# Performance work log

Hardware: AMD Instinct MI355X
Metric: run time of the kernel (lower is better)

Reference implementation:

```python
import jax, jax.numpy as jnp
import numpy as np

BSZ, L, D = 64, 128, 2048


def setup_inputs() -> dict:
    key = jax.random.key(0)
    k1, k2, k3 = jax.random.split(key, 3)
    encoder_output = jax.random.normal(k1, (BSZ, L, D), dtype=jnp.float32)
    # ragged turn lengths in [2, L]; prefix mask like torch turn_lengths = mask.sum(1)
    lengths = jax.random.randint(k2, (BSZ,), 2, L + 1)
    mask = (jnp.arange(L)[None, :] < lengths[:, None]).astype(jnp.int32)
    W = jax.random.normal(k3, (2 * D, 2), dtype=jnp.float32) * (1.0 / np.sqrt(2 * D))
    b = jnp.zeros((2,), dtype=jnp.float32)
    return {"encoder_output": encoder_output, "mask": mask, "W": W, "b": b}


def reference(encoder_output, mask, W, b):
    bsz, max_len, d = encoder_output.shape
    turn_lengths = jnp.sum(mask, axis=1)  # [bsz]
    # con_fc(concat(h_j, h_k)) == h_j @ W[:d] + h_k @ W[d:] + b  (exact split of the linear)
    left = jnp.einsum('bld,dc->blc', encoder_output, W[:d])   # [b, L, 2]
    right = jnp.einsum('bld,dc->blc', encoder_output, W[d:])  # [b, L, 2]
    logits = left[:, :, None, :] + right[:, None, :, :] + b   # [b, L(j), L(k), 2]
    j = jnp.arange(max_len)[:, None]
    k = jnp.arange(max_len)[None, :]
    # pairs gathered by torch loops: k < j < turn_lengths[i]; label 1 iff k == j-1
    valid = (k < j) & (j < turn_lengths[:, None, None])        # [b, L, L]
    labels = (k == j - 1).astype(jnp.int32)                    # [L, L]
    logp = jax.nn.log_softmax(logits, axis=-1)                 # [b, L, L, 2]
    nll = -jnp.take_along_axis(
        logp, jnp.broadcast_to(labels[None, :, :, None], (bsz, max_len, max_len, 1)), axis=-1
    )[..., 0]                                                  # [b, L, L]
    n_valid = jnp.sum(valid)
    dli_loss = jnp.sum(jnp.where(valid, nll, 0.0)) / jnp.maximum(n_valid, 1).astype(nll.dtype)
    return dli_loss
```

## Files before the change

### kernel.cpp

```cpp
#include <hip/hip_runtime.h>

#define BSZ 64
#define LMAX 128
#define DIM 2048
#define NPOS (BSZ * LMAX)

struct Ctrl {
    float accum;
    int   count;
    int   done2;
};

__global__ __launch_bounds__(512, 6) void proj_kernel(
        const float* __restrict__ enc,
        const float* __restrict__ W,
        float* __restrict__ proj,
        Ctrl* __restrict__ ctrl) {
    if (blockIdx.x == 0 && threadIdx.x == 0) {
        ctrl->accum = 0.f; ctrl->count = 0; ctrl->done2 = 0;
    }

    const int tid  = threadIdx.x;
    const int wid  = tid >> 6;
    const int lane = tid & 63;
    const int quad = wid >> 2;
    const int qw   = wid & 3;
    const int p0   = (blockIdx.x * 2 + quad) * 4;

    const float4* __restrict__ W4 = (const float4*)W;
    float4 wl0[2], wl1[2], wr0[2], wr1[2];
    #pragma unroll
    for (int it = 0; it < 2; ++it) {
        const int idx = qw * 128 + it * 64 + lane;
        wl0[it] = W4[idx * 2];
        wl1[it] = W4[idx * 2 + 1];
        wr0[it] = W4[1024 + idx * 2];
        wr1[it] = W4[1024 + idx * 2 + 1];
    }

    const float4* __restrict__ h4 = (const float4*)enc;
    const size_t base = (size_t)p0 * (DIM / 4) + qw * 128 + lane;

    float4 hA0 = h4[base];
    float4 hA1 = h4[base + 64];

    float* __restrict__ projf = proj + (size_t)qw * NPOS * 4;

    #pragma unroll
    for (int q = 0; q < 4; ++q) {
        float4 hB0, hB1;
        if (q < 3) {
            const size_t nb = base + (size_t)(q + 1) * (DIM / 4);
            hB0 = h4[nb];
            hB1 = h4[nb + 64];
        }
        float a0, a1, a2, a3;
        a0 = hA0.x * wl0[0].x + hA0.y * wl0[0].z + hA0.z * wl1[0].x + hA0.w * wl1[0].z
           + hA1.x * wl0[1].x + hA1.y * wl0[1].z + hA1.z * wl1[1].x + hA1.w * wl1[1].z;
        a1 = hA0.x * wl0[0].y + hA0.y * wl0[0].w + hA0.z * wl1[0].y + hA0.w * wl1[0].w
           + hA1.x * wl0[1].y + hA1.y * wl0[1].w + hA1.z * wl1[1].y + hA1.w * wl1[1].w;
        a2 = hA0.x * wr0[0].x + hA0.y * wr0[0].z + hA0.z * wr1[0].x + hA0.w * wr1[0].z
           + hA1.x * wr0[1].x + hA1.y * wr0[1].z + hA1.z * wr1[1].x + hA1.w * wr1[1].z;
        a3 = hA0.x * wr0[0].y + hA0.y * wr0[0].w + hA0.z * wr1[0].y + hA0.w * wr1[0].w
           + hA1.x * wr0[1].y + hA1.y * wr0[1].w + hA1.z * wr1[1].y + hA1.w * wr1[1].w;

        const bool o1 = (lane & 1);
        const float r1 = __shfl_xor(o1 ? a0 : a1, 1);
        float s = (o1 ? a1 : a0) + r1;
        const float r2 = __shfl_xor(o1 ? a2 : a3, 1);
        float t = (o1 ? a3 : a2) + r2;
        const bool o2 = (lane & 2);
        const float r3 = __shfl_xor(o2 ? s : t, 2);
        float u = (o2 ? t : s) + r3;
        u += __shfl_xor(u, 4);
        u += __shfl_xor(u, 8);
        u += __shfl_xor(u, 16);
        u += __shfl_xor(u, 32);
        if (lane < 4) projf[(size_t)(p0 + q) * 4 + lane] = u;

        if (q < 3) { hA0 = hB0; hA1 = hB1; }
    }
}

__global__ __launch_bounds__(256) void loss_kernel(
        const int* __restrict__ mask,
        const float* __restrict__ proj,
        const float* __restrict__ bias,
        Ctrl* __restrict__ ctrl,
        float* __restrict__ out) {
    __shared__ float4 s_proj[LMAX];
    __shared__ float  s_w[4];
    __shared__ int    s_m[4];

    const int b   = blockIdx.x >> 2;
    const int q   = blockIdx.x & 3;
    const int tid = threadIdx.x;

    const float4* proj4 = (const float4*)proj;
    if (tid < LMAX) {
        const float4 pa = proj4[0 * NPOS + b * LMAX + tid];
        const float4 pb = proj4[1 * NPOS + b * LMAX + tid];
        const float4 pc = proj4[2 * NPOS + b * LMAX + tid];
        const float4 pd = proj4[3 * NPOS + b * LMAX + tid];
        float4 v;
        v.x = (pa.x + pb.x) + (pc.x + pd.x);
        v.y = (pa.y + pb.y) + (pc.y + pd.y);
        v.z = (pa.z + pb.z) + (pc.z + pd.z);
        v.w = (pa.w + pb.w) + (pc.w + pd.w);
        s_proj[tid] = v;
    }

    int m = (tid < LMAX) ? mask[b * LMAX + tid] : 0;
    #pragma unroll
    for (int off = 32; off >= 1; off >>= 1) m += __shfl_xor(m, off);
    if ((tid & 63) == 0) s_m[tid >> 6] = m;
    __syncthreads();

    const int   T  = s_m[0] + s_m[1] + s_m[2] + s_m[3];
    const float b0 = bias[0];
    const float b1 = bias[1];

    float local = 0.f;
    const int tmax = T << 7;
    for (int t = q * 256 + tid; t < tmax; t += 1024) {
        const int j = t >> 7;
        const int k = t & (LMAX - 1);
        if (k < j) {
            const float4 pj = s_proj[j];
            const float4 pk = s_proj[k];
            const float l0 = pj.x + pk.z + b0;
            const float l1 = pj.y + pk.w + b1;
            const bool  pos = (k == j - 1);
            const float d  = pos ? (l0 - l1) : (l1 - l0);
            local += fmaxf(d, 0.f) + __logf(1.f + __expf(-fabsf(d)));
        }
    }

    #pragma unroll
    for (int off = 32; off >= 1; off >>= 1) local += __shfl_xor(local, off);
    if ((tid & 63) == 0) s_w[tid >> 6] = local;
    __syncthreads();

    if (tid == 0) {
        atomicAdd(&ctrl->accum, s_w[0] + s_w[1] + s_w[2] + s_w[3]);
        if (q == 0) atomicAdd(&ctrl->count, T * (T - 1) / 2);
        __threadfence();
        const int prev = atomicAdd(&ctrl->done2, 1);
        if (prev == 4 * BSZ - 1) {
            const float s = atomicAdd(&ctrl->accum, 0.0f);
            const int   c = atomicAdd(&ctrl->count, 0);
            out[0] = s / (float)(c > 1 ? c : 1);
        }
    }
}

extern "C" void kernel_launch(void* const* d_in, const int* in_sizes, int n_in,
                              void* d_out, int out_size, void* d_ws, size_t ws_size,
                              hipStream_t stream) {
    const float* enc  = (const float*)d_in[0];
    const int*   mask = (const int*)d_in[1];
    const float* W    = (const float*)d_in[2];
    const float* bias = (const float*)d_in[3];
    float* out = (float*)d_out;

    float* proj = (float*)d_ws;
    Ctrl*  ctrl = (Ctrl*)((char*)d_ws + 4 * NPOS * 16);

    proj_kernel<<<NPOS / 8, 512, 0, stream>>>(enc, W, proj, ctrl);
    loss_kernel<<<4 * BSZ, 256, 0, stream>>>(mask, proj, bias, ctrl, out);
}
```

Baseline: 26.93 us.

## Fuse projection and loss into one kernel with per-batch completion flags

Merges the projection and loss kernels into a single launch. The first 1024 blocks compute projections and bump a per-batch counter; 64 tail blocks (one per batch, 512 threads) spin on their batch's counter and then compute the loss. A tiny init kernel zeroes the control block, so there are still two launches. The aim is to overlap the loss with projection work and avoid the gap between kernels. The spin-wait depends on block scheduling order, since tail blocks have higher indices, and the loss work per block grows as it drops from four blocks per batch to one.

```diff
diff --git a/kernel.cpp b/kernel.cpp
--- a/kernel.cpp
+++ b/kernel.cpp
@@ -4,97 +4,115 @@
 #define LMAX 128
 #define DIM 2048
 #define NPOS (BSZ * LMAX)
+#define NPROJ_BLOCKS 1024
+#define NTAIL BSZ
 
 struct Ctrl {
     float accum;
     int   count;
     int   done2;
+    int   pad[13];
+    int   done[BSZ * 16];
 };
 
-__global__ __launch_bounds__(512, 6) void proj_kernel(
+__global__ void init_kernel(Ctrl* __restrict__ ctrl) {
+    int* p = (int*)ctrl;
+    const int n = sizeof(Ctrl) / 4;
+    for (int i = threadIdx.x; i < n; i += 256) p[i] = 0;
+}
+
+__global__ __launch_bounds__(512, 6) void fused_kernel(
         const float* __restrict__ enc,
         const float* __restrict__ W,
+        const int* __restrict__ mask,
+        const float* __restrict__ bias,
         float* __restrict__ proj,
-        Ctrl* __restrict__ ctrl) {
-    if (blockIdx.x == 0 && threadIdx.x == 0) {
-        ctrl->accum = 0.f; ctrl->count = 0; ctrl->done2 = 0;
+        Ctrl* __restrict__ ctrl,
+        float* __restrict__ out) {
+    const int tid = threadIdx.x;
+
+    if (blockIdx.x < NPROJ_BLOCKS) {
+        const int wid  = tid >> 6;
+        const int lane = tid & 63;
+        const int quad = wid >> 2;
+        const int qw   = wid & 3;
+        const int p0   = (blockIdx.x * 2 + quad) * 4;
+
+        const float4* __restrict__ W4 = (const float4*)W;
+        float4 wl0[2], wl1[2], wr0[2], wr1[2];
+        #pragma unroll
+        for (int it = 0; it < 2; ++it) {
+            const int idx = qw * 128 + it * 64 + lane;
+            wl0[it] = W4[idx * 2];
+            wl1[it] = W4[idx * 2 + 1];
+            wr0[it] = W4[1024 + idx * 2];
+            wr1[it] = W4[1024 + idx * 2 + 1];
+        }
+
+        const float4* __restrict__ h4 = (const float4*)enc;
+        const size_t base = (size_t)p0 * (DIM / 4) + qw * 128 + lane;
+
+        float4 hA0 = h4[base];
+        float4 hA1 = h4[base + 64];
+
+        float* __restrict__ projf = proj + (size_t)qw * NPOS * 4;
+
+        #pragma unroll
+        for (int q = 0; q < 4; ++q) {
+            float4 hB0, hB1;
+            if (q < 3) {
+                const size_t nb = base + (size_t)(q + 1) * (DIM / 4);
+                hB0 = h4[nb];
+                hB1 = h4[nb + 64];
+            }
+            float a0, a1, a2, a3;
+            a0 = hA0.x * wl0[0].x + hA0.y * wl0[0].z + hA0.z * wl1[0].x + hA0.w * wl1[0].z
+               + hA1.x * wl0[1].x + hA1.y * wl0[1].z + hA1.z * wl1[1].x + hA1.w * wl1[1].z;
+            a1 = hA0.x * wl0[0].y + hA0.y * wl0[0].w + hA0.z * wl1[0].y + hA0.w * wl1[0].w
+               + hA1.x * wl0[1].y + hA1.y * wl0[1].w + hA1.z * wl1[1].y + hA1.w * wl1[1].w;
+            a2 = hA0.x * wr0[0].x + hA0.y * wr0[0].z + hA0.z * wr1[0].x + hA0.w * wr1[0].z
+               + hA1.x * wr0[1].x + hA1.y * wr0[1].z + hA1.z * wr1[1].x + hA1.w * wr1[1].z;
+            a3 = hA0.x * wr0[0].y + hA0.y * wr0[0].w + hA0.z * wr1[0].y + hA0.w * wr1[0].w
+               + hA1.x * wr0[1].y + hA1.y * wr0[1].w + hA1.z * wr1[1].y + hA1.w * wr1[1].w;
+
+            const bool o1 = (lane & 1);
+            const float r1 = __shfl_xor(o1 ? a0 : a1, 1);
+            float s = (o1 ? a1 : a0) + r1;
+            const float r2 = __shfl_xor(o1 ? a2 : a3, 1);
+            float t = (o1 ? a3 : a2) + r2;
+            const bool o2 = (lane & 2);
+            const float r3 = __shfl_xor(o2 ? s : t, 2);
+            float u = (o2 ? t : s) + r3;
+            u += __shfl_xor(u, 4);
+            u += __shfl_xor(u, 8);
+            u += __shfl_xor(u, 16);
+            u += __shfl_xor(u, 32);
+            if (lane < 4) projf[(size_t)(p0 + q) * 4 + lane] = u;
+
+            if (q < 3) { hA0 = hB0; hA1 = hB1; }
+        }
+
+        __syncthreads();
+        if (tid == 0) {
+            __threadfence();
+            atomicAdd(&ctrl->done[(blockIdx.x >> 4) * 16], 1);
+        }
+        return;
     }
 
-    const int tid  = threadIdx.x;
-    const int wid  = tid >> 6;
+    __shared__ float4 s_proj[LMAX];
+    __shared__ float  s_w[8];
+    __shared__ int    s_m[8];
+
+    const int b    = blockIdx.x - NPROJ_BLOCKS;
     const int lane = tid & 63;
-    const int quad = wid >> 2;
-    const int qw   = wid & 3;
-    const int p0   = (blockIdx.x * 2 + quad) * 4;
 
-    const float4* __restrict__ W4 = (const float4*)W;
-    float4 wl0[2], wl1[2], wr0[2], wr1[2];
-    #pragma unroll
-    for (int it = 0; it < 2; ++it) {
-        const int idx = qw * 128 + it * 64 + lane;
-        wl0[it] = W4[idx * 2];
-        wl1[it] = W4[idx * 2 + 1];
-        wr0[it] = W4[1024 + idx * 2];
-        wr1[it] = W4[1024 + idx * 2 + 1];
+    if (tid == 0) {
+        while (atomicAdd(&ctrl->done[b * 16], 0) < 16)
+            __builtin_amdgcn_s_sleep(1);
+        __threadfence();
     }
-
-    const float4* __restrict__ h4 = (const float4*)enc;
-    const size_t base = (size_t)p0 * (DIM / 4) + qw * 128 + lane;
-
-    float4 hA0 = h4[base];
-    float4 hA1 = h4[base + 64];
-
-    float* __restrict__ projf = proj + (size_t)qw * NPOS * 4;
-
-    #pragma unroll
-    for (int q = 0; q < 4; ++q) {
-        float4 hB0, hB1;
-        if (q < 3) {
-            const size_t nb = base + (size_t)(q + 1) * (DIM / 4);
-            hB0 = h4[nb];
-            hB1 = h4[nb + 64];
-        }
-        float a0, a1, a2, a3;
-        a0 = hA0.x * wl0[0].x + hA0.y * wl0[0].z + hA0.z * wl1[0].x + hA0.w * wl1[0].z
-           + hA1.x * wl0[1].x + hA1.y * wl0[1].z + hA1.z * wl1[1].x + hA1.w * wl1[1].z;
-        a1 = hA0.x * wl0[0].y + hA0.y * wl0[0].w + hA0.z * wl1[0].y + hA0.w * wl1[0].w
-           + hA1.x * wl0[1].y + hA1.y * wl0[1].w + hA1.z * wl1[1].y + hA1.w * wl1[1].w;
-        a2 = hA0.x * wr0[0].x + hA0.y * wr0[0].z + hA0.z * wr1[0].x + hA0.w * wr1[0].z
-           + hA1.x * wr0[1].x + hA1.y * wr0[1].z + hA1.z * wr1[1].x + hA1.w * wr1[1].z;
-        a3 = hA0.x * wr0[0].y + hA0.y * wr0[0].w + hA0.z * wr1[0].y + hA0.w * wr1[0].w
-           + hA1.x * wr0[1].y + hA1.y * wr0[1].w + hA1.z * wr1[1].y + hA1.w * wr1[1].w;
-
-        const bool o1 = (lane & 1);
-        const float r1 = __shfl_xor(o1 ? a0 : a1, 1);
-        float s = (o1 ? a1 : a0) + r1;
-        const float r2 = __shfl_xor(o1 ? a2 : a3, 1);
-        float t = (o1 ? a3 : a2) + r2;
-        const bool o2 = (lane & 2);
-        const float r3 = __shfl_xor(o2 ? s : t, 2);
-        float u = (o2 ? t : s) + r3;
-        u += __shfl_xor(u, 4);
-        u += __shfl_xor(u, 8);
-        u += __shfl_xor(u, 16);
-        u += __shfl_xor(u, 32);
-        if (lane < 4) projf[(size_t)(p0 + q) * 4 + lane] = u;
-
-        if (q < 3) { hA0 = hB0; hA1 = hB1; }
-    }
-}
-
-__global__ __launch_bounds__(256) void loss_kernel(
-        const int* __restrict__ mask,
-        const float* __restrict__ proj,
-        const float* __restrict__ bias,
-        Ctrl* __restrict__ ctrl,
-        float* __restrict__ out) {
-    __shared__ float4 s_proj[LMAX];
-    __shared__ float  s_w[4];
-    __shared__ int    s_m[4];
-
-    const int b   = blockIdx.x >> 2;
-    const int q   = blockIdx.x & 3;
-    const int tid = threadIdx.x;
+    __syncthreads();
 
     const float4* proj4 = (const float4*)proj;
     if (tid < LMAX) {
@@ -113,16 +131,18 @@
     int m = (tid < LMAX) ? mask[b * LMAX + tid] : 0;
     #pragma unroll
     for (int off = 32; off >= 1; off >>= 1) m += __shfl_xor(m, off);
-    if ((tid & 63) == 0) s_m[tid >> 6] = m;
+    if (lane == 0) s_m[tid >> 6] = m;
     __syncthreads();
 
-    const int   T  = s_m[0] + s_m[1] + s_m[2] + s_m[3];
+    int T = 0;
+    #pragma unroll
+    for (int w = 0; w < 8; ++w) T += s_m[w];
     const float b0 = bias[0];
     const float b1 = bias[1];
 
     float local = 0.f;
     const int tmax = T << 7;
-    for (int t = q * 256 + tid; t < tmax; t += 1024) {
+    for (int t = tid; t < tmax; t += 512) {
         const int j = t >> 7;
         const int k = t & (LMAX - 1);
         if (k < j) {
@@ -138,18 +158,21 @@
 
     #pragma unroll
     for (int off = 32; off >= 1; off >>= 1) local += __shfl_xor(local, off);
-    if ((tid & 63) == 0) s_w[tid >> 6] = local;
+    if (lane == 0) s_w[tid >> 6] = local;
     __syncthreads();
 
     if (tid == 0) {
-        atomicAdd(&ctrl->accum, s_w[0] + s_w[1] + s_w[2] + s_w[3]);
-        if (q == 0) atomicAdd(&ctrl->count, T * (T - 1) / 2);
+        float s = 0.f;
+        #pragma unroll
+        for (int w = 0; w < 8; ++w) s += s_w[w];
+        atomicAdd(&ctrl->accum, s);
+        atomicAdd(&ctrl->count, T * (T - 1) / 2);
         __threadfence();
         const int prev = atomicAdd(&ctrl->done2, 1);
-        if (prev == 4 * BSZ - 1) {
-            const float s = atomicAdd(&ctrl->accum, 0.0f);
-            const int   c = atomicAdd(&ctrl->count, 0);
-            out[0] = s / (float)(c > 1 ? c : 1);
+        if (prev == NTAIL - 1) {
+            const float sum = atomicAdd(&ctrl->accum, 0.0f);
+            const int   c   = atomicAdd(&ctrl->count, 0);
+            out[0] = sum / (float)(c > 1 ? c : 1);
         }
     }
 }
@@ -166,6 +189,7 @@
     float* proj = (float*)d_ws;
     Ctrl*  ctrl = (Ctrl*)((char*)d_ws + 4 * NPOS * 16);
 
-    proj_kernel<<<NPOS / 8, 512, 0, stream>>>(enc, W, proj, ctrl);
-    loss_kernel<<<4 * BSZ, 256, 0, stream>>>(mask, proj, bias, ctrl, out);
+    init_kernel<<<1, 256, 0, stream>>>(ctrl);
+    fused_kernel<<<NPROJ_BLOCKS + NTAIL, 512, 0, stream>>>(
+        enc, W, mask, bias, proj, ctrl, out);
 }
```

Result: slower. 64.64 us (+140.0%).

## Fuse projection and loss into one per-batch kernel with shared-memory partials

Applied to the files above, without the earlier changes.

Merges the projection and pairwise-loss kernels into a single kernel with one 1024-thread block per batch row. Per-position projections go into shared memory, so the global proj workspace and the second launch are gone, and control reset moves to a hipMemsetAsync. In exchange, only 64 blocks run on a many-CU GPU. Each wave also walks 32 rows serially with single-step prefetch, which may limit memory parallelism for streaming the 64 MB input.

```diff
diff --git a/kernel.cpp b/kernel.cpp
--- a/kernel.cpp
+++ b/kernel.cpp
@@ -3,7 +3,6 @@
 #define BSZ 64
 #define LMAX 128
 #define DIM 2048
-#define NPOS (BSZ * LMAX)
 
 struct Ctrl {
     float accum;
@@ -11,21 +10,24 @@
     int   done2;
 };
 
-__global__ __launch_bounds__(512, 6) void proj_kernel(
+__global__ __launch_bounds__(1024) void mono_kernel(
         const float* __restrict__ enc,
         const float* __restrict__ W,
-        float* __restrict__ proj,
-        Ctrl* __restrict__ ctrl) {
-    if (blockIdx.x == 0 && threadIdx.x == 0) {
-        ctrl->accum = 0.f; ctrl->count = 0; ctrl->done2 = 0;
-    }
+        const int* __restrict__ mask,
+        const float* __restrict__ bias,
+        Ctrl* __restrict__ ctrl,
+        float* __restrict__ out) {
+    __shared__ float  s_part[4][LMAX][4];
+    __shared__ float4 s_proj[LMAX];
+    __shared__ float  s_w[16];
+    __shared__ int    s_m[2];
 
+    const int b    = blockIdx.x;
     const int tid  = threadIdx.x;
     const int wid  = tid >> 6;
     const int lane = tid & 63;
-    const int quad = wid >> 2;
+    const int g    = wid >> 2;
     const int qw   = wid & 3;
-    const int p0   = (blockIdx.x * 2 + quad) * 4;
 
     const float4* __restrict__ W4 = (const float4*)W;
     float4 wl0[2], wl1[2], wr0[2], wr1[2];
@@ -38,18 +40,23 @@
         wr1[it] = W4[1024 + idx * 2 + 1];
     }
 
+    if (tid < LMAX) {
+        int m = mask[b * LMAX + tid];
+        #pragma unroll
+        for (int off = 32; off >= 1; off >>= 1) m += __shfl_xor(m, off);
+        if (lane == 0) s_m[wid] = m;
+    }
+
     const float4* __restrict__ h4 = (const float4*)enc;
-    const size_t base = (size_t)p0 * (DIM / 4) + qw * 128 + lane;
+    const int    pl0  = g * 32;
+    const size_t base = ((size_t)(b * LMAX + pl0)) * (DIM / 4) + qw * 128 + lane;
 
     float4 hA0 = h4[base];
     float4 hA1 = h4[base + 64];
 
-    float* __restrict__ projf = proj + (size_t)qw * NPOS * 4;
-
-    #pragma unroll
-    for (int q = 0; q < 4; ++q) {
+    for (int q = 0; q < 32; ++q) {
         float4 hB0, hB1;
-        if (q < 3) {
+        if (q < 31) {
             const size_t nb = base + (size_t)(q + 1) * (DIM / 4);
             hB0 = h4[nb];
             hB1 = h4[nb + 64];
@@ -76,53 +83,33 @@
         u += __shfl_xor(u, 8);
         u += __shfl_xor(u, 16);
         u += __shfl_xor(u, 32);
-        if (lane < 4) projf[(size_t)(p0 + q) * 4 + lane] = u;
+        if (lane < 4) s_part[qw][pl0 + q][lane] = u;
 
-        if (q < 3) { hA0 = hB0; hA1 = hB1; }
+        if (q < 31) { hA0 = hB0; hA1 = hB1; }
     }
-}
+    __syncthreads();
 
-__global__ __launch_bounds__(256) void loss_kernel(
-        const int* __restrict__ mask,
-        const float* __restrict__ proj,
-        const float* __restrict__ bias,
-        Ctrl* __restrict__ ctrl,
-        float* __restrict__ out) {
-    __shared__ float4 s_proj[LMAX];
-    __shared__ float  s_w[4];
-    __shared__ int    s_m[4];
-
-    const int b   = blockIdx.x >> 2;
-    const int q   = blockIdx.x & 3;
-    const int tid = threadIdx.x;
-
-    const float4* proj4 = (const float4*)proj;
     if (tid < LMAX) {
-        const float4 pa = proj4[0 * NPOS + b * LMAX + tid];
-        const float4 pb = proj4[1 * NPOS + b * LMAX + tid];
-        const float4 pc = proj4[2 * NPOS + b * LMAX + tid];
-        const float4 pd = proj4[3 * NPOS + b * LMAX + tid];
         float4 v;
-        v.x = (pa.x + pb.x) + (pc.x + pd.x);
-        v.y = (pa.y + pb.y) + (pc.y + pd.y);
-        v.z = (pa.z + pb.z) + (pc.z + pd.z);
-        v.w = (pa.w + pb.w) + (pc.w + pd.w);
+        const float4 p0 = *(const float4*)s_part[0][tid];
+        const float4 p1 = *(const float4*)s_part[1][tid];
+        const float4 p2 = *(const float4*)s_part[2][tid];
+        const float4 p3 = *(const float4*)s_part[3][tid];
+        v.x = (p0.x + p1.x) + (p2.x + p3.x);
+        v.y = (p0.y + p1.y) + (p2.y + p3.y);
+        v.z = (p0.z + p1.z) + (p2.z + p3.z);
+        v.w = (p0.w + p1.w) + (p2.w + p3.w);
         s_proj[tid] = v;
     }
-
-    int m = (tid < LMAX) ? mask[b * LMAX + tid] : 0;
-    #pragma unroll
-    for (int off = 32; off >= 1; off >>= 1) m += __shfl_xor(m, off);
-    if ((tid & 63) == 0) s_m[tid >> 6] = m;
     __syncthreads();
 
-    const int   T  = s_m[0] + s_m[1] + s_m[2] + s_m[3];
+    const int   T  = s_m[0] + s_m[1];
     const float b0 = bias[0];
     const float b1 = bias[1];
 
     float local = 0.f;
     const int tmax = T << 7;
-    for (int t = q * 256 + tid; t < tmax; t += 1024) {
+    for (int t = tid; t < tmax; t += 1024) {
         const int j = t >> 7;
         const int k = t & (LMAX - 1);
         if (k < j) {
@@ -135,21 +122,23 @@
             local += fmaxf(d, 0.f) + __logf(1.f + __expf(-fabsf(d)));
         }
     }
-
     #pragma unroll
     for (int off = 32; off >= 1; off >>= 1) local += __shfl_xor(local, off);
-    if ((tid & 63) == 0) s_w[tid >> 6] = local;
+    if (lane == 0) s_w[wid] = local;
     __syncthreads();
 
     if (tid == 0) {
-        atomicAdd(&ctrl->accum, s_w[0] + s_w[1] + s_w[2] + s_w[3]);
-        if (q == 0) atomicAdd(&ctrl->count, T * (T - 1) / 2);
+        float s = 0.f;
+        #pragma unroll
+        for (int w = 0; w < 16; ++w) s += s_w[w];
+        atomicAdd(&ctrl->accum, s);
+        atomicAdd(&ctrl->count, T * (T - 1) / 2);
         __threadfence();
         const int prev = atomicAdd(&ctrl->done2, 1);
-        if (prev == 4 * BSZ - 1) {
-            const float s = atomicAdd(&ctrl->accum, 0.0f);
-            const int   c = atomicAdd(&ctrl->count, 0);
-            out[0] = s / (float)(c > 1 ? c : 1);
+        if (prev == BSZ - 1) {
+            const float sum = atomicAdd(&ctrl->accum, 0.0f);
+            const int   c   = atomicAdd(&ctrl->count, 0);
+            out[0] = sum / (float)(c > 1 ? c : 1);
         }
     }
 }
@@ -163,9 +152,8 @@
     const float* bias = (const float*)d_in[3];
     float* out = (float*)d_out;
 
-    float* proj = (float*)d_ws;
-    Ctrl*  ctrl = (Ctrl*)((char*)d_ws + 4 * NPOS * 16);
+    Ctrl* ctrl = (Ctrl*)d_ws;
 
-    proj_kernel<<<NPOS / 8, 512, 0, stream>>>(enc, W, proj, ctrl);
-    loss_kernel<<<4 * BSZ, 256, 0, stream>>>(mask, proj, bias, ctrl, out);
+    hipMemsetAsync(ctrl, 0, sizeof(Ctrl), stream);
+    mono_kernel<<<BSZ, 1024, 0, stream>>>(enc, W, mask, bias, ctrl, out);
 }
```

Measured after the change: 30.03 us. 11.5% more time.

## Split projection reduction across eight wave slices, issue all row loads upfront

Applied to the files above, without the earlier changes.

Each wave now covers one 256-wide slice of the hidden dimension across all eight positions of the block, instead of four waves per four positions. All eight row loads are issued before any compute, which raises memory-level parallelism per thread. The partial projections grow from four to eight per position, so the loss kernel sums eight partials and the workspace doubles. Register use rises from holding eight float4 rows, and the launch-bounds occupancy hint drops from 6 to 4 blocks per CU.

```diff
diff --git a/kernel.cpp b/kernel.cpp
--- a/kernel.cpp
+++ b/kernel.cpp
@@ -11,7 +11,7 @@
     int   done2;
 };
 
-__global__ __launch_bounds__(512, 6) void proj_kernel(
+__global__ __launch_bounds__(512, 4) void proj_kernel(
         const float* __restrict__ enc,
         const float* __restrict__ W,
         float* __restrict__ proj,
@@ -21,48 +21,32 @@
     }
 
     const int tid  = threadIdx.x;
-    const int wid  = tid >> 6;
+    const int e    = tid >> 6;
     const int lane = tid & 63;
-    const int quad = wid >> 2;
-    const int qw   = wid & 3;
-    const int p0   = (blockIdx.x * 2 + quad) * 4;
+    const int p0   = blockIdx.x * 8;
+    const int idx  = e * 64 + lane;
 
     const float4* __restrict__ W4 = (const float4*)W;
-    float4 wl0[2], wl1[2], wr0[2], wr1[2];
-    #pragma unroll
-    for (int it = 0; it < 2; ++it) {
-        const int idx = qw * 128 + it * 64 + lane;
-        wl0[it] = W4[idx * 2];
-        wl1[it] = W4[idx * 2 + 1];
-        wr0[it] = W4[1024 + idx * 2];
-        wr1[it] = W4[1024 + idx * 2 + 1];
-    }
+    const float4 wl0 = W4[idx * 2];
+    const float4 wl1 = W4[idx * 2 + 1];
+    const float4 wr0 = W4[1024 + idx * 2];
+    const float4 wr1 = W4[1024 + idx * 2 + 1];
 
     const float4* __restrict__ h4 = (const float4*)enc;
-    const size_t base = (size_t)p0 * (DIM / 4) + qw * 128 + lane;
+    const size_t base = (size_t)p0 * (DIM / 4) + idx;
+    float4 h[8];
+    #pragma unroll
+    for (int p = 0; p < 8; ++p) h[p] = h4[base + (size_t)p * (DIM / 4)];
 
-    float4 hA0 = h4[base];
-    float4 hA1 = h4[base + 64];
-
-    float* __restrict__ projf = proj + (size_t)qw * NPOS * 4;
+    float* __restrict__ projf = proj + (size_t)e * NPOS * 4;
 
     #pragma unroll
-    for (int q = 0; q < 4; ++q) {
-        float4 hB0, hB1;
-        if (q < 3) {
-            const size_t nb = base + (size_t)(q + 1) * (DIM / 4);
-            hB0 = h4[nb];
-            hB1 = h4[nb + 64];
-        }
-        float a0, a1, a2, a3;
-        a0 = hA0.x * wl0[0].x + hA0.y * wl0[0].z + hA0.z * wl1[0].x + hA0.w * wl1[0].z
-           + hA1.x * wl0[1].x + hA1.y * wl0[1].z + hA1.z * wl1[1].x + hA1.w * wl1[1].z;
-        a1 = hA0.x * wl0[0].y + hA0.y * wl0[0].w + hA0.z * wl1[0].y + hA0.w * wl1[0].w
-           + hA1.x * wl0[1].y + hA1.y * wl0[1].w + hA1.z * wl1[1].y + hA1.w * wl1[1].w;
-        a2 = hA0.x * wr0[0].x + hA0.y * wr0[0].z + hA0.z * wr1[0].x + hA0.w * wr1[0].z
-           + hA1.x * wr0[1].x + hA1.y * wr0[1].z + hA1.z * wr1[1].x + hA1.w * wr1[1].z;
-        a3 = hA0.x * wr0[0].y + hA0.y * wr0[0].w + hA0.z * wr1[0].y + hA0.w * wr1[0].w
-           + hA1.x * wr0[1].y + hA1.y * wr0[1].w + hA1.z * wr1[1].y + hA1.w * wr1[1].w;
+    for (int p = 0; p < 8; ++p) {
+        const float4 hp = h[p];
+        float a0 = hp.x * wl0.x + hp.y * wl0.z + hp.z * wl1.x + hp.w * wl1.z;
+        float a1 = hp.x * wl0.y + hp.y * wl0.w + hp.z * wl1.y + hp.w * wl1.w;
+        float a2 = hp.x * wr0.x + hp.y * wr0.z + hp.z * wr1.x + hp.w * wr1.z;
+        float a3 = hp.x * wr0.y + hp.y * wr0.w + hp.z * wr1.y + hp.w * wr1.w;
 
         const bool o1 = (lane & 1);
         const float r1 = __shfl_xor(o1 ? a0 : a1, 1);
@@ -76,9 +60,7 @@
         u += __shfl_xor(u, 8);
         u += __shfl_xor(u, 16);
         u += __shfl_xor(u, 32);
-        if (lane < 4) projf[(size_t)(p0 + q) * 4 + lane] = u;
-
-        if (q < 3) { hA0 = hB0; hA1 = hB1; }
+        if (lane < 4) projf[(size_t)(p0 + p) * 4 + lane] = u;
     }
 }
 
@@ -98,15 +80,13 @@
 
     const float4* proj4 = (const float4*)proj;
     if (tid < LMAX) {
-        const float4 pa = proj4[0 * NPOS + b * LMAX + tid];
-        const float4 pb = proj4[1 * NPOS + b * LMAX + tid];
-        const float4 pc = proj4[2 * NPOS + b * LMAX + tid];
-        const float4 pd = proj4[3 * NPOS + b * LMAX + tid];
-        float4 v;
-        v.x = (pa.x + pb.x) + (pc.x + pd.x);
-        v.y = (pa.y + pb.y) + (pc.y + pd.y);
-        v.z = (pa.z + pb.z) + (pc.z + pd.z);
-        v.w = (pa.w + pb.w) + (pc.w + pd.w);
+        float x = 0.f, y = 0.f, z = 0.f, w = 0.f;
+        #pragma unroll
+        for (int e = 0; e < 8; ++e) {
+            const float4 pe = proj4[e * NPOS + b * LMAX + tid];
+            x += pe.x; y += pe.y; z += pe.z; w += pe.w;
+        }
+        float4 v; v.x = x; v.y = y; v.z = z; v.w = w;
         s_proj[tid] = v;
     }
 
@@ -164,7 +144,7 @@
     float* out = (float*)d_out;
 
     float* proj = (float*)d_ws;
-    Ctrl*  ctrl = (Ctrl*)((char*)d_ws + 4 * NPOS * 16);
+    Ctrl*  ctrl = (Ctrl*)((char*)d_ws + 8 * NPOS * 16);
 
     proj_kernel<<<NPOS / 8, 512, 0, stream>>>(enc, W, proj, ctrl);
     loss_kernel<<<4 * BSZ, 256, 0, stream>>>(mask, proj, bias, ctrl, out);
```

Result: slower. 27.95 us (+3.8%).
